# Optimization experiments

Measured on AMD Instinct MI355X. Metric: run time of the kernel, lower is better.

The kernel has to match this reference:

```python
import jax, jax.numpy as jnp
import numpy as np

B, SRC_LEN, TGT_LEN = 8, 512, 64
D, NUM_HEADS = 512, 8
VOCAB, EXT_VOCAB = 32000, 2048


def setup_inputs() -> dict:
    key = jax.random.key(0)
    ks = jax.random.split(key, 11)
    s = 1.0 / np.sqrt(D).astype(np.float32)
    return {
        "logits": jax.random.normal(ks[0], (B, TGT_LEN, VOCAB), jnp.float32),
        "extended_vocab_ids": jax.random.randint(ks[1], (B, SRC_LEN), 0, VOCAB + EXT_VOCAB),
        "src_subtokens": jax.random.normal(ks[2], (B, SRC_LEN, D), jnp.float32),
        "src_padding": jax.random.randint(ks[3], (B, SRC_LEN), 0, 2).astype(bool),
        "tgt_subtokens": jax.random.normal(ks[4], (B, TGT_LEN, D), jnp.float32),
        "w_q": jax.random.normal(ks[5], (D, D), jnp.float32) * s,
        "b_q": jnp.zeros((D,), jnp.float32),
        "w_k": jax.random.normal(ks[6], (D, D), jnp.float32) * s,
        "b_k": jnp.zeros((D,), jnp.float32),
        "w_copy": jax.random.normal(ks[7], (D,), jnp.float32) * s,
        "b_copy": jnp.zeros((), jnp.float32),
        "len_vocab": VOCAB,
        "max_len_extended_vocab": EXT_VOCAB,
    }


def reference(logits, extended_vocab_ids, src_subtokens, src_padding, tgt_subtokens,
              w_q, b_q, w_k, b_k, w_copy, b_copy, len_vocab, max_len_extended_vocab):
    Bv, T, V = logits.shape
    S = src_subtokens.shape[1]
    Dh = D // NUM_HEADS
    v_total = len_vocab + max_len_extended_vocab

    # generation/copy gate: sigmoid(Linear(tgt)) -> (B, T, 1)
    copy_prob = jax.nn.sigmoid(tgt_subtokens @ w_copy + b_copy)[..., None]

    # SimpleMHA: q/k projections, scaled dot-product, pad-mask, softmax, mean over heads
    q = (tgt_subtokens @ w_q + b_q).reshape(Bv, T, NUM_HEADS, Dh)
    k = (src_subtokens @ w_k + b_k).reshape(Bv, S, NUM_HEADS, Dh)
    scores = jnp.einsum('bthd,bshd->bhts', q, k) / np.sqrt(Dh).astype(np.float32)
    scores = jnp.where(src_padding[:, None, None, :], -jnp.inf, scores)
    attn_dist = jax.nn.softmax(scores, axis=-1).mean(axis=1)  # (B, T, S)

    # one-hot scatter + bmm in the original == scatter-add of attention into vocab slots
    def scat(a, ids):  # a: (T, S), ids: (S,)
        return jnp.zeros((T, v_total), a.dtype).at[:, ids].add(a)
    attention = jax.vmap(scat)(attn_dist, extended_vocab_ids)  # (B, T, v_total)

    eps = jnp.finfo(jnp.float32).eps
    pointer_log_probs = jnp.log(jnp.where(attention == 0, eps, attention))

    dec = jax.nn.log_softmax(logits, axis=-1)
    dec = jnp.pad(dec, ((0, 0), (0, 0), (0, max_len_extended_vocab)),
                  constant_values=-np.inf)

    fmin = jnp.finfo(jnp.float32).min
    p0 = dec + jnp.log(1.0 - copy_prob)
    p1 = pointer_log_probs + jnp.log(copy_prob)
    p0 = jnp.where(p0 == -jnp.inf, fmin, p0)
    p1 = jnp.where(p1 == -jnp.inf, fmin, p1)
    return jnp.logaddexp(p0, p1)
```

## Files before the change

### kernel.cpp

```cpp
#include <hip/hip_runtime.h>
#include <math.h>

#define BATCH 8
#define SRC 512
#define TGT 64
#define DMODEL 512
#define NHEAD 8
#define DH 64
#define VOCAB 32000
#define EXTV 2048
#define VTOT 34048

#define LOG_EPS -15.9423851529f
#define FMIN_   -3.402823466e38f

typedef short short8 __attribute__((ext_vector_type(8)));
typedef float f32x4 __attribute__((ext_vector_type(4)));
typedef unsigned short us4 __attribute__((ext_vector_type(4)));

__device__ __forceinline__ float wave_reduce_sum(float v){
  for (int off = 32; off; off >>= 1) v += __shfl_xor(v, off, 64);
  return v;
}
__device__ __forceinline__ float wave_reduce_max(float v){
  for (int off = 32; off; off >>= 1) v = fmaxf(v, __shfl_xor(v, off, 64));
  return v;
}
__device__ __forceinline__ unsigned short f2bf(float x){
  unsigned u = __float_as_uint(x);
  unsigned r = (u + 0x7FFFu + ((u >> 16) & 1u)) >> 16;
  return (unsigned short)r;
}

__global__ __launch_bounds__(256) void detect_mask_kernel(
    const unsigned int* __restrict__ pad_words, int* __restrict__ flag)
{
  __shared__ int s_bad;
  int tid = threadIdx.x;
  if (tid == 0) s_bad = 0;
  __syncthreads();
  int bad = 0;
  for (int i = tid; i < 1024; i += 256)
    if (pad_words[i] > 1u) bad = 1;
  if (bad) atomicOr(&s_bad, 1);
  __syncthreads();
  if (tid == 0) *flag = s_bad;
}

__global__ __launch_bounds__(256) void f2bf_kernel(
    const float4* __restrict__ in, unsigned short* __restrict__ out, int n4)
{
  int i = blockIdx.x * 256 + threadIdx.x;
  if (i >= n4) return;
  float4 x = in[i];
  us4 o = { f2bf(x.x), f2bf(x.y), f2bf(x.z), f2bf(x.w) };
  *reinterpret_cast<us4*>(&out[4 * i]) = o;
}

__global__ __launch_bounds__(256) void wt_kernel(
    const float* __restrict__ W, unsigned short* __restrict__ Wt)
{
  __shared__ float t[32][33];
  int k0 = blockIdx.x * 32, n0 = blockIdx.y * 32;
  int tx = threadIdx.x & 31, ty = threadIdx.x >> 5;
  #pragma unroll
  for (int i = 0; i < 4; i++)
    t[ty + 8 * i][tx] = W[(size_t)(k0 + ty + 8 * i) * DMODEL + n0 + tx];
  __syncthreads();
  #pragma unroll
  for (int i = 0; i < 4; i++)
    Wt[(size_t)(n0 + ty + 8 * i) * DMODEL + k0 + tx] = f2bf(t[tx][ty + 8 * i]);
}

template<int KT>
__global__ __launch_bounds__(256) void mfma_gemm(
    const unsigned short* __restrict__ A, const unsigned short* __restrict__ Wt,
    const float* __restrict__ bias, float* __restrict__ C)
{
  __shared__ __align__(16) unsigned short As[128 * 40];
  __shared__ __align__(16) unsigned short Bs[64 * 40];
  int tid = threadIdx.x, lane = tid & 63, wv = tid >> 6;
  int wm = wv >> 1, wn = wv & 1;
  int m0 = blockIdx.x * 128, n0 = blockIdx.y * 64;
  int ml = lane & 15, kq = lane >> 4;
  f32x4 acc[4][2] = {};

  int r = tid >> 2, c = tid & 3;
  for (int k0 = 0; k0 < DMODEL; k0 += 32){
    *reinterpret_cast<short8*>(&As[r * 40 + c * 8]) =
        *reinterpret_cast<const short8*>(&A[(size_t)(m0 + r) * DMODEL + k0 + c * 8]);
    *reinterpret_cast<short8*>(&As[(r + 64) * 40 + c * 8]) =
        *reinterpret_cast<const short8*>(&A[(size_t)(m0 + r + 64) * DMODEL + k0 + c * 8]);
    *reinterpret_cast<short8*>(&Bs[r * 40 + c * 8]) =
        *reinterpret_cast<const short8*>(&Wt[(size_t)(n0 + r) * DMODEL + k0 + c * 8]);
    __syncthreads();
    short8 af[4], bf[2];
    #pragma unroll
    for (int mi = 0; mi < 4; mi++)
      af[mi] = *reinterpret_cast<const short8*>(&As[(wm * 64 + mi * 16 + ml) * 40 + kq * 8]);
    #pragma unroll
    for (int ni = 0; ni < 2; ni++)
      bf[ni] = *reinterpret_cast<const short8*>(&Bs[(wn * 32 + ni * 16 + ml) * 40 + kq * 8]);
    #pragma unroll
    for (int mi = 0; mi < 4; mi++)
      #pragma unroll
      for (int ni = 0; ni < 2; ni++){
        if (KT)
          acc[mi][ni] = __builtin_amdgcn_mfma_f32_16x16x32_bf16(bf[ni], af[mi], acc[mi][ni], 0, 0, 0);
        else
          acc[mi][ni] = __builtin_amdgcn_mfma_f32_16x16x32_bf16(af[mi], bf[ni], acc[mi][ni], 0, 0, 0);
      }
    __syncthreads();
  }

  #pragma unroll
  for (int mi = 0; mi < 4; mi++)
    #pragma unroll
    for (int ni = 0; ni < 2; ni++)
      #pragma unroll
      for (int reg = 0; reg < 4; reg++){
        if (KT){
          int m = m0 + wm * 64 + mi * 16 + ml;
          int n = n0 + wn * 32 + ni * 16 + kq * 4 + reg;
          C[((size_t)(m >> 9) * DMODEL + n) * SRC + (m & 511)] = acc[mi][ni][reg] + bias[n];
        } else {
          int m = m0 + wm * 64 + mi * 16 + kq * 4 + reg;
          int n = n0 + wn * 32 + ni * 16 + ml;
          C[(size_t)m * DMODEL + n] = acc[mi][ni][reg] + bias[n];
        }
      }
}

__global__ __launch_bounds__(512) void attn_kernel(
    const float* __restrict__ q, const float* __restrict__ kt,
    const unsigned char* __restrict__ pad_u8, const int* __restrict__ pad_i32,
    const int* __restrict__ padflag, float* __restrict__ attn)
{
  __shared__ float qs[DMODEL];
  __shared__ float sc[NHEAD][SRC];
  int row = (blockIdx.x & 7) * TGT + (blockIdx.x >> 3);
  int b = blockIdx.x & 7;
  int tid = threadIdx.x, lane = tid & 63, h = tid >> 6;
  int isU8 = *padflag;
  qs[tid] = q[(size_t)row * DMODEL + tid];
  __syncthreads();

  const float* ktb = kt + (size_t)(b * NHEAD + h) * DH * SRC;
  float dot[8] = {};
  #pragma unroll 4
  for (int d = 0; d < DH; d++){
    float qv = qs[h * DH + d];
    const float* rowp = ktb + (size_t)d * SRC + lane;
    #pragma unroll
    for (int i = 0; i < 8; i++)
      dot[i] += rowp[64 * i] * qv;
  }

  int sbase = b * SRC;
  float sv[8];
  float m = -INFINITY;
  #pragma unroll
  for (int i = 0; i < 8; i++){
    int s = lane + 64 * i;
    int masked = isU8 ? (pad_u8[sbase + s] != 0) : (pad_i32[sbase + s] != 0);
    sv[i] = masked ? -INFINITY : dot[i] * 0.125f;
    m = fmaxf(m, sv[i]);
  }
  m = wave_reduce_max(m);
  float sum = 0.f;
  #pragma unroll
  for (int i = 0; i < 8; i++){ sv[i] = __expf(sv[i] - m); sum += sv[i]; }
  sum = wave_reduce_sum(sum);
  float inv = 1.f / sum;
  #pragma unroll
  for (int i = 0; i < 8; i++) sc[h][lane + 64 * i] = sv[i] * inv;
  __syncthreads();

  #pragma unroll
  for (int s0 = 0; s0 < SRC; s0 += 512){
    int s = s0 + tid;
    float a = 0.f;
    #pragma unroll
    for (int hh = 0; hh < NHEAD; hh++) a += sc[hh][s];
    attn[(size_t)row * SRC + s] = a * 0.125f;
  }
}

__global__ __launch_bounds__(512) void vocab_kernel(
    const float* __restrict__ logits, const int* __restrict__ ids,
    const float* __restrict__ attn, const float* __restrict__ tgt,
    const float* __restrict__ w_copy, const float* __restrict__ b_copy,
    float* __restrict__ out)
{
  __shared__ float redA[8], redB[8];
  __shared__ int   hid[1024];
  __shared__ float hval[1024];
  int row = blockIdx.x;
  int b = row >> 6;
  int tid = threadIdx.x, lane = tid & 63, wv = tid >> 6;

  float g = tgt[(size_t)row * DMODEL + tid] * w_copy[tid];
  g = wave_reduce_sum(g);
  if (lane == 0) redA[wv] = g;
  for (int i = tid; i < 1024; i += 512){ hid[i] = -1; hval[i] = 0.f; }
  __syncthreads();
  float z = b_copy[0];
  #pragma unroll
  for (int i = 0; i < 8; i++) z += redA[i];
  float eu = __expf(-z);
  float Lg = __logf(1.f + eu);
  float lc = -Lg;
  float l1c = -z - Lg;

  const float4* lr4 = reinterpret_cast<const float4*>(logits + (size_t)row * VOCAB);
  float m = -INFINITY, sm = 0.f;
  for (int v4 = tid; v4 < VOCAB / 4; v4 += 512){
    float4 x = lr4[v4];
    float mx4 = fmaxf(fmaxf(x.x, x.y), fmaxf(x.z, x.w));
    if (mx4 > m){ sm *= __expf(m - mx4); m = mx4; }
    sm += __expf(x.x - m) + __expf(x.y - m) + __expf(x.z - m) + __expf(x.w - m);
  }
  for (int off = 32; off; off >>= 1){
    float m2 = __shfl_xor(m, off, 64), s2 = __shfl_xor(sm, off, 64);
    float M = fmaxf(m, m2);
    sm = sm * __expf(m - M) + s2 * __expf(m2 - M);
    m = M;
  }
  __syncthreads();
  if (lane == 0){ redA[wv] = m; redB[wv] = sm; }
  __syncthreads();
  float mx = -INFINITY, se = 0.f;
  #pragma unroll
  for (int i = 0; i < 8; i++){
    float mi = redA[i], si = redB[i];
    float M = fmaxf(mx, mi);
    se = se * __expf(mx - M) + si * __expf(mi - M);
    mx = M;
  }
  float lse = __logf(se);

  float p1c = LOG_EPS + lc;
  float c2 = mx + lse - l1c + p1c;
  float4* o4 = reinterpret_cast<float4*>(out + (size_t)row * VTOT);
  for (int v4 = tid; v4 < VTOT / 4; v4 += 512){
    float4 rr;
    if (v4 < VOCAB / 4){
      float4 x = lr4[v4];
      rr.x = p1c + __logf(1.f + __expf(x.x - c2));
      rr.y = p1c + __logf(1.f + __expf(x.y - c2));
      rr.z = p1c + __logf(1.f + __expf(x.z - c2));
      rr.w = p1c + __logf(1.f + __expf(x.w - c2));
    } else {
      rr.x = rr.y = rr.z = rr.w = p1c;
    }
    o4[v4] = rr;
  }

  {
    int id = ids[b * SRC + tid];
    float val = attn[(size_t)row * SRC + tid];
    unsigned h = (((unsigned)id * 2654435761u) >> 22) & 1023;
    while (true){
      int cur = atomicCAS(&hid[h], -1, id);
      if (cur == -1 || cur == id) break;
      h = (h + 1) & 1023;
    }
    atomicAdd(&hval[h], val);
  }
  __syncthreads();
  for (int i = tid; i < 1024; i += 512){
    int id = hid[i];
    if (id < 0) continue;
    float a = hval[i];
    float plp = (a == 0.f) ? LOG_EPS : __logf(a);
    float p1 = plp + lc;
    float p0 = (id < VOCAB) ? (logits[(size_t)row * VOCAB + id] - mx - lse) + l1c : FMIN_;
    float hi = fmaxf(p0, p1), lo = fminf(p0, p1);
    out[(size_t)row * VTOT + id] = hi + __logf(1.f + __expf(lo - hi));
  }
}

extern "C" void kernel_launch(void* const* d_in, const int* in_sizes, int n_in,
                              void* d_out, int out_size, void* d_ws, size_t ws_size,
                              hipStream_t stream)
{
  const float*         logits = (const float*)d_in[0];
  const int*           ids    = (const int*)d_in[1];
  const float*         src    = (const float*)d_in[2];
  const unsigned char* pad_u8 = (const unsigned char*)d_in[3];
  const int*           pad_i32= (const int*)d_in[3];
  const float*         tgt    = (const float*)d_in[4];
  const float*         w_q    = (const float*)d_in[5];
  const float*         b_q    = (const float*)d_in[6];
  const float*         w_k    = (const float*)d_in[7];
  const float*         b_k    = (const float*)d_in[8];
  const float*         w_copy = (const float*)d_in[9];
  const float*         b_copy = (const float*)d_in[10];
  float* out = (float*)d_out;

  float* q      = (float*)d_ws;
  float* kt     = q    + BATCH * TGT * DMODEL;
  float* attn   = kt   + BATCH * SRC * DMODEL;
  int*   padflag= (int*)(attn + BATCH * TGT * SRC);
  unsigned short* src_bf = (unsigned short*)(padflag + 4);
  unsigned short* tgt_bf = src_bf + BATCH * SRC * DMODEL;
  unsigned short* wq_t   = tgt_bf + BATCH * TGT * DMODEL;
  unsigned short* wk_t   = wq_t   + DMODEL * DMODEL;

  detect_mask_kernel<<<dim3(1), 256, 0, stream>>>((const unsigned int*)d_in[3], padflag);
  f2bf_kernel<<<dim3(BATCH * SRC * DMODEL / 4 / 256), 256, 0, stream>>>(
      (const float4*)src, src_bf, BATCH * SRC * DMODEL / 4);
  f2bf_kernel<<<dim3(BATCH * TGT * DMODEL / 4 / 256), 256, 0, stream>>>(
      (const float4*)tgt, tgt_bf, BATCH * TGT * DMODEL / 4);
  wt_kernel<<<dim3(16, 16), 256, 0, stream>>>(w_q, wq_t);
  wt_kernel<<<dim3(16, 16), 256, 0, stream>>>(w_k, wk_t);

  mfma_gemm<0><<<dim3(BATCH * TGT / 128, DMODEL / 64), 256, 0, stream>>>(
      tgt_bf, wq_t, b_q, q);
  mfma_gemm<1><<<dim3(BATCH * SRC / 128, DMODEL / 64), 256, 0, stream>>>(
      src_bf, wk_t, b_k, kt);

  attn_kernel<<<dim3(BATCH * TGT), 512, 0, stream>>>(q, kt, pad_u8, pad_i32, padflag, attn);
  vocab_kernel<<<dim3(BATCH * TGT), 512, 0, stream>>>(
      logits, ids, attn, tgt, w_copy, b_copy, out);
}
```

Baseline: 217.8 us.

## Fuse bf16 conversion into projection GEMM, merge launches, widen vocab blocks

The separate float-to-bf16 conversion kernels for src/tgt are removed; the projection GEMM now loads fp32 activations and converts them to bf16 while staging into shared memory. The Q and K GEMMs are merged into one launch, and the two weight transposes into one 3D-grid launch. This cuts the launch count and an intermediate bf16 round trip. The vocab kernel also goes from 512 to 1024 threads per block, which may change occupancy.

```diff
diff --git a/kernel.cpp b/kernel.cpp
--- a/kernel.cpp
+++ b/kernel.cpp
@@ -16,7 +16,6 @@
 
 typedef short short8 __attribute__((ext_vector_type(8)));
 typedef float f32x4 __attribute__((ext_vector_type(4)));
-typedef unsigned short us4 __attribute__((ext_vector_type(4)));
 
 __device__ __forceinline__ float wave_reduce_sum(float v){
   for (int off = 32; off; off >>= 1) v += __shfl_xor(v, off, 64);
@@ -47,20 +46,13 @@
   if (tid == 0) *flag = s_bad;
 }
 
-__global__ __launch_bounds__(256) void f2bf_kernel(
-    const float4* __restrict__ in, unsigned short* __restrict__ out, int n4)
-{
-  int i = blockIdx.x * 256 + threadIdx.x;
-  if (i >= n4) return;
-  float4 x = in[i];
-  us4 o = { f2bf(x.x), f2bf(x.y), f2bf(x.z), f2bf(x.w) };
-  *reinterpret_cast<us4*>(&out[4 * i]) = o;
-}
-
-__global__ __launch_bounds__(256) void wt_kernel(
-    const float* __restrict__ W, unsigned short* __restrict__ Wt)
+__global__ __launch_bounds__(256) void wt2_kernel(
+    const float* __restrict__ Wq, const float* __restrict__ Wk,
+    unsigned short* __restrict__ Wq_t, unsigned short* __restrict__ Wk_t)
 {
   __shared__ float t[32][33];
+  const float* W = blockIdx.z ? Wk : Wq;
+  unsigned short* Wt = blockIdx.z ? Wk_t : Wq_t;
   int k0 = blockIdx.x * 32, n0 = blockIdx.y * 32;
   int tx = threadIdx.x & 31, ty = threadIdx.x >> 5;
   #pragma unroll
@@ -72,27 +64,39 @@
     Wt[(size_t)(n0 + ty + 8 * i) * DMODEL + k0 + tx] = f2bf(t[tx][ty + 8 * i]);
 }
 
-template<int KT>
-__global__ __launch_bounds__(256) void mfma_gemm(
-    const unsigned short* __restrict__ A, const unsigned short* __restrict__ Wt,
-    const float* __restrict__ bias, float* __restrict__ C)
+__global__ __launch_bounds__(256) void proj_kernel(
+    const float* __restrict__ tgt, const float* __restrict__ src,
+    const unsigned short* __restrict__ wq_t, const unsigned short* __restrict__ wk_t,
+    const float* __restrict__ b_q, const float* __restrict__ b_k,
+    float* __restrict__ q, float* __restrict__ kt)
 {
   __shared__ __align__(16) unsigned short As[128 * 40];
   __shared__ __align__(16) unsigned short Bs[64 * 40];
+  int bx = blockIdx.x;
+  bool kmode = bx >= 4;
+  const float* A = kmode ? src : tgt;
+  const unsigned short* Wt = kmode ? wk_t : wq_t;
+  const float* bias = kmode ? b_k : b_q;
+  int m0 = (kmode ? bx - 4 : bx) * 128;
+  int n0 = blockIdx.y * 64;
   int tid = threadIdx.x, lane = tid & 63, wv = tid >> 6;
   int wm = wv >> 1, wn = wv & 1;
-  int m0 = blockIdx.x * 128, n0 = blockIdx.y * 64;
   int ml = lane & 15, kq = lane >> 4;
   f32x4 acc[4][2] = {};
 
   int r = tid >> 2, c = tid & 3;
   for (int k0 = 0; k0 < DMODEL; k0 += 32){
-    *reinterpret_cast<short8*>(&As[r * 40 + c * 8]) =
-        *reinterpret_cast<const short8*>(&A[(size_t)(m0 + r) * DMODEL + k0 + c * 8]);
-    *reinterpret_cast<short8*>(&As[(r + 64) * 40 + c * 8]) =
-        *reinterpret_cast<const short8*>(&A[(size_t)(m0 + r + 64) * DMODEL + k0 + c * 8]);
+    #pragma unroll
+    for (int half = 0; half < 2; half++){
+      const float* ap = &A[(size_t)(m0 + r + 64 * half) * DMODEL + k0 + c * 8];
+      float4 x0 = *reinterpret_cast<const float4*>(ap);
+      float4 x1 = *reinterpret_cast<const float4*>(ap + 4);
+      short8 s8 = { (short)f2bf(x0.x), (short)f2bf(x0.y), (short)f2bf(x0.z), (short)f2bf(x0.w),
+                    (short)f2bf(x1.x), (short)f2bf(x1.y), (short)f2bf(x1.z), (short)f2bf(x1.w) };
+      *reinterpret_cast<short8*>(&As[(r + 64 * half) * 40 + c * 8]) = s8;
+    }
     *reinterpret_cast<short8*>(&Bs[r * 40 + c * 8]) =
-        *reinterpret_cast<const short8*>(&Wt[(size_t)(n0 + r) * DMODEL + k0 + c * 8]);
+        *reinterpret_cast<const short8*>(&Wt[(size_t)(n0 + (r & 63)) * DMODEL + k0 + c * 8]);
     __syncthreads();
     short8 af[4], bf[2];
     #pragma unroll
@@ -101,15 +105,19 @@
     #pragma unroll
     for (int ni = 0; ni < 2; ni++)
       bf[ni] = *reinterpret_cast<const short8*>(&Bs[(wn * 32 + ni * 16 + ml) * 40 + kq * 8]);
-    #pragma unroll
-    for (int mi = 0; mi < 4; mi++)
+    if (kmode){
       #pragma unroll
-      for (int ni = 0; ni < 2; ni++){
-        if (KT)
+      for (int mi = 0; mi < 4; mi++)
+        #pragma unroll
+        for (int ni = 0; ni < 2; ni++)
           acc[mi][ni] = __builtin_amdgcn_mfma_f32_16x16x32_bf16(bf[ni], af[mi], acc[mi][ni], 0, 0, 0);
-        else
+    } else {
+      #pragma unroll
+      for (int mi = 0; mi < 4; mi++)
+        #pragma unroll
+        for (int ni = 0; ni < 2; ni++)
           acc[mi][ni] = __builtin_amdgcn_mfma_f32_16x16x32_bf16(af[mi], bf[ni], acc[mi][ni], 0, 0, 0);
-      }
+    }
     __syncthreads();
   }
 
@@ -119,14 +127,14 @@
     for (int ni = 0; ni < 2; ni++)
       #pragma unroll
       for (int reg = 0; reg < 4; reg++){
-        if (KT){
+        if (kmode){
           int m = m0 + wm * 64 + mi * 16 + ml;
           int n = n0 + wn * 32 + ni * 16 + kq * 4 + reg;
-          C[((size_t)(m >> 9) * DMODEL + n) * SRC + (m & 511)] = acc[mi][ni][reg] + bias[n];
+          kt[((size_t)(m >> 9) * DMODEL + n) * SRC + (m & 511)] = acc[mi][ni][reg] + bias[n];
         } else {
           int m = m0 + wm * 64 + mi * 16 + kq * 4 + reg;
           int n = n0 + wn * 32 + ni * 16 + ml;
-          C[(size_t)m * DMODEL + n] = acc[mi][ni][reg] + bias[n];
+          q[(size_t)m * DMODEL + n] = acc[mi][ni][reg] + bias[n];
         }
       }
 }
@@ -186,27 +194,27 @@
   }
 }
 
-__global__ __launch_bounds__(512) void vocab_kernel(
+__global__ __launch_bounds__(1024) void vocab_kernel(
     const float* __restrict__ logits, const int* __restrict__ ids,
     const float* __restrict__ attn, const float* __restrict__ tgt,
     const float* __restrict__ w_copy, const float* __restrict__ b_copy,
     float* __restrict__ out)
 {
-  __shared__ float redA[8], redB[8];
+  __shared__ float redA[16], redB[16];
   __shared__ int   hid[1024];
   __shared__ float hval[1024];
   int row = blockIdx.x;
   int b = row >> 6;
   int tid = threadIdx.x, lane = tid & 63, wv = tid >> 6;
 
-  float g = tgt[(size_t)row * DMODEL + tid] * w_copy[tid];
+  float g = (tid < DMODEL) ? tgt[(size_t)row * DMODEL + tid] * w_copy[tid] : 0.f;
   g = wave_reduce_sum(g);
   if (lane == 0) redA[wv] = g;
-  for (int i = tid; i < 1024; i += 512){ hid[i] = -1; hval[i] = 0.f; }
+  hid[tid] = -1; hval[tid] = 0.f;
   __syncthreads();
   float z = b_copy[0];
   #pragma unroll
-  for (int i = 0; i < 8; i++) z += redA[i];
+  for (int i = 0; i < 16; i++) z += redA[i];
   float eu = __expf(-z);
   float Lg = __logf(1.f + eu);
   float lc = -Lg;
@@ -214,7 +222,7 @@
 
   const float4* lr4 = reinterpret_cast<const float4*>(logits + (size_t)row * VOCAB);
   float m = -INFINITY, sm = 0.f;
-  for (int v4 = tid; v4 < VOCAB / 4; v4 += 512){
+  for (int v4 = tid; v4 < VOCAB / 4; v4 += 1024){
     float4 x = lr4[v4];
     float mx4 = fmaxf(fmaxf(x.x, x.y), fmaxf(x.z, x.w));
     if (mx4 > m){ sm *= __expf(m - mx4); m = mx4; }
@@ -231,7 +239,7 @@
   __syncthreads();
   float mx = -INFINITY, se = 0.f;
   #pragma unroll
-  for (int i = 0; i < 8; i++){
+  for (int i = 0; i < 16; i++){
     float mi = redA[i], si = redB[i];
     float M = fmaxf(mx, mi);
     se = se * __expf(mx - M) + si * __expf(mi - M);
@@ -242,7 +250,7 @@
   float p1c = LOG_EPS + lc;
   float c2 = mx + lse - l1c + p1c;
   float4* o4 = reinterpret_cast<float4*>(out + (size_t)row * VTOT);
-  for (int v4 = tid; v4 < VTOT / 4; v4 += 512){
+  for (int v4 = tid; v4 < VTOT / 4; v4 += 1024){
     float4 rr;
     if (v4 < VOCAB / 4){
       float4 x = lr4[v4];
@@ -256,7 +264,7 @@
     o4[v4] = rr;
   }
 
-  {
+  if (tid < SRC){
     int id = ids[b * SRC + tid];
     float val = attn[(size_t)row * SRC + tid];
     unsigned h = (((unsigned)id * 2654435761u) >> 22) & 1023;
@@ -268,15 +276,16 @@
     atomicAdd(&hval[h], val);
   }
   __syncthreads();
-  for (int i = tid; i < 1024; i += 512){
-    int id = hid[i];
-    if (id < 0) continue;
-    float a = hval[i];
-    float plp = (a == 0.f) ? LOG_EPS : __logf(a);
-    float p1 = plp + lc;
-    float p0 = (id < VOCAB) ? (logits[(size_t)row * VOCAB + id] - mx - lse) + l1c : FMIN_;
-    float hi = fmaxf(p0, p1), lo = fminf(p0, p1);
-    out[(size_t)row * VTOT + id] = hi + __logf(1.f + __expf(lo - hi));
+  {
+    int id = hid[tid];
+    if (id >= 0){
+      float a = hval[tid];
+      float plp = (a == 0.f) ? LOG_EPS : __logf(a);
+      float p1 = plp + lc;
+      float p0 = (id < VOCAB) ? (logits[(size_t)row * VOCAB + id] - mx - lse) + l1c : FMIN_;
+      float hi = fmaxf(p0, p1), lo = fminf(p0, p1);
+      out[(size_t)row * VTOT + id] = hi + __logf(1.f + __expf(lo - hi));
+    }
   }
 }
 
@@ -302,25 +311,14 @@
   float* kt     = q    + BATCH * TGT * DMODEL;
   float* attn   = kt   + BATCH * SRC * DMODEL;
   int*   padflag= (int*)(attn + BATCH * TGT * SRC);
-  unsigned short* src_bf = (unsigned short*)(padflag + 4);
-  unsigned short* tgt_bf = src_bf + BATCH * SRC * DMODEL;
-  unsigned short* wq_t   = tgt_bf + BATCH * TGT * DMODEL;
-  unsigned short* wk_t   = wq_t   + DMODEL * DMODEL;
+  unsigned short* wq_t = (unsigned short*)(padflag + 4);
+  unsigned short* wk_t = wq_t + DMODEL * DMODEL;
 
   detect_mask_kernel<<<dim3(1), 256, 0, stream>>>((const unsigned int*)d_in[3], padflag);
-  f2bf_kernel<<<dim3(BATCH * SRC * DMODEL / 4 / 256), 256, 0, stream>>>(
-      (const float4*)src, src_bf, BATCH * SRC * DMODEL / 4);
-  f2bf_kernel<<<dim3(BATCH * TGT * DMODEL / 4 / 256), 256, 0, stream>>>(
-      (const float4*)tgt, tgt_bf, BATCH * TGT * DMODEL / 4);
-  wt_kernel<<<dim3(16, 16), 256, 0, stream>>>(w_q, wq_t);
-  wt_kernel<<<dim3(16, 16), 256, 0, stream>>>(w_k, wk_t);
-
-  mfma_gemm<0><<<dim3(BATCH * TGT / 128, DMODEL / 64), 256, 0, stream>>>(
-      tgt_bf, wq_t, b_q, q);
-  mfma_gemm<1><<<dim3(BATCH * SRC / 128, DMODEL / 64), 256, 0, stream>>>(
-      src_bf, wk_t, b_k, kt);
-
+  wt2_kernel<<<dim3(16, 16, 2), 256, 0, stream>>>(w_q, w_k, wq_t, wk_t);
+  proj_kernel<<<dim3(4 + BATCH * SRC / 128, DMODEL / 64), 256, 0, stream>>>(
+      tgt, src, wq_t, wk_t, b_q, b_k, q, kt);
   attn_kernel<<<dim3(BATCH * TGT), 512, 0, stream>>>(q, kt, pad_u8, pad_i32, padflag, attn);
-  vocab_kernel<<<dim3(BATCH * TGT), 512, 0, stream>>>(
+  vocab_kernel<<<dim3(BATCH * TGT), 1024, 0, stream>>>(
       logits, ids, attn, tgt, w_copy, b_copy, out);
 }
```

Measured after the change: 208.6 us. 1.04x faster.
